# Performance work log

Hardware: AMD Instinct MI355X
Metric: run time of the kernel (lower is better)

Reference implementation:

```python
import jax, jax.numpy as jnp
import numpy as np

VALUES_PER_ITEM = 4  # 2-bit packed -> 4 values per uint8


def setup_inputs() -> dict:
    key = jax.random.key(0)
    k1, k2, k3 = jax.random.split(key, 3)
    x = jax.random.normal(k1, (4, 4096, 2048), dtype=jnp.float32)
    # packed uint8 weights, stored as int32 with values in [0, 256)
    weight_packed = jax.random.randint(k2, (512, 2048), 0, 256, dtype=jnp.int32)
    weight_scale = jnp.ones((1,), dtype=jnp.float32)
    bias = jax.random.normal(k3, (2048,), dtype=jnp.float32) * 0.01
    return {"x": x, "weight_packed": weight_packed,
            "weight_scale": weight_scale, "bias": bias}


def unpack_weights_bitnet(packed, dtype):
    # packed: [out//4, in]. HF BitNet layout: group i occupies rows
    # [i*out//4 : (i+1)*out//4], extracted from bits (2i, 2i+1), minus 1.
    parts = [((packed >> (2 * i)) & 3) for i in range(VALUES_PER_ITEM)]
    return jnp.concatenate(parts, axis=0).astype(dtype) - 1.0  # [out, in]


def activation_quant(x, num_bits=8):
    qn = -(2 ** (num_bits - 1))          # -128
    qp = 2 ** (num_bits - 1) - 1         # 127
    amax = jnp.clip(jnp.max(jnp.abs(x), axis=-1, keepdims=True), 1e-5, None)
    scale = qp / amax                    # per-token scale, [..., 1]
    # round-half-to-even matches torch .round(); keep in float (int8-valued)
    xq = jnp.clip(jnp.round(x * scale), qn, qp)
    return xq, scale


def reference(x, weight_packed, weight_scale, bias):
    w = unpack_weights_bitnet(weight_packed, x.dtype)  # [out, in]
    xq, in_scale = activation_quant(x)                 # [b,s,in], [b,s,1]
    y = jnp.einsum('bsd,od->bso', xq, w)               # int8-valued GEMM in fp
    y = y / (weight_scale * in_scale)                  # rescale
    return y + bias
```

## Files before the change

kernel.cpp:

```cpp
#include <hip/hip_runtime.h>
#include <stdint.h>


typedef __attribute__((ext_vector_type(4)))  int int4v;
typedef __attribute__((ext_vector_type(16))) int int16v;

#define GLOBAL_AS __attribute__((address_space(1)))
#define LDS_AS    __attribute__((address_space(3)))

static constexpr int MK = 2048;
static constexpr int NN = 2048;
static constexpr int MM = 16384;

__global__ void quant_kernel(const float* __restrict__ x,
                             const float* __restrict__ wscale,
                             signed char* __restrict__ xq,
                             float* __restrict__ rf) {
    const int m = blockIdx.x;
    const int t = threadIdx.x;
    const float4* xr = (const float4*)(x + (size_t)m * MK);
    float4 v0 = xr[t];
    float4 v1 = xr[t + 256];
    float amax = fmaxf(fmaxf(fabsf(v0.x), fabsf(v0.y)),
                       fmaxf(fabsf(v0.z), fabsf(v0.w)));
    amax = fmaxf(amax, fmaxf(fmaxf(fabsf(v1.x), fabsf(v1.y)),
                             fmaxf(fabsf(v1.z), fabsf(v1.w))));
    #pragma unroll
    for (int off = 32; off >= 1; off >>= 1)
        amax = fmaxf(amax, __shfl_xor(amax, off));
    __shared__ float smax[4];
    if ((t & 63) == 0) smax[t >> 6] = amax;
    __syncthreads();
    float a0 = fmaxf(fmaxf(smax[0], smax[1]), fmaxf(smax[2], smax[3]));
    a0 = fmaxf(a0, 1e-5f);
    const float scale = 127.0f / a0;
    if (t == 0) rf[m] = a0 / (127.0f * wscale[0]);

    auto q = [&](float f) -> int {
        float r = rintf(f * scale);
        r = fminf(fmaxf(r, -128.0f), 127.0f);
        return (int)r;
    };
    int p0 = (q(v0.x) & 255) | ((q(v0.y) & 255) << 8) |
             ((q(v0.z) & 255) << 16) | ((q(v0.w) & 255) << 24);
    int p1 = (q(v1.x) & 255) | ((q(v1.y) & 255) << 8) |
             ((q(v1.z) & 255) << 16) | ((q(v1.w) & 255) << 24);
    int* xqr = (int*)(xq + (size_t)m * MK);
    xqr[t]       = p0;
    xqr[t + 256] = p1;
}

__global__ void unpack_kernel(const int* __restrict__ packed,
                              signed char* __restrict__ W) {
    const int idx = blockIdx.x * 256 + threadIdx.x;
    const int r  = idx >> 9;
    const int kq = idx & 511;
    const int4 p = ((const int4*)packed)[idx];
    int* Wi = (int*)W;
    #pragma unroll
    for (int i = 0; i < 4; i++) {
        const int sh = 2 * i;
        int b0 = ((((p.x >> sh) & 3) - 1) & 255);
        int b1 = ((((p.y >> sh) & 3) - 1) & 255);
        int b2 = ((((p.z >> sh) & 3) - 1) & 255);
        int b3 = ((((p.w >> sh) & 3) - 1) & 255);
        Wi[(i * 512 + r) * 512 + kq] = b0 | (b1 << 8) | (b2 << 16) | (b3 << 24);
    }
}

#define WAITV(N) asm volatile("s_waitcnt vmcnt(" #N ")" ::: "memory")
#define BAR() do { __builtin_amdgcn_s_barrier(); \
                   __builtin_amdgcn_sched_barrier(0); } while (0)

__device__ __forceinline__ void stage_half(const signed char* __restrict__ src,
                                           int row0, int k0, int h, int ss,
                                           unsigned char* plane,
                                           int wave, int lane) {
    const int csrc = (((lane & 7) ^ (lane >> 3)) << 4);
    #pragma unroll
    for (int j = 0; j < 2; ++j) {
        const int rw = wave * 16 + j * 8 + (lane >> 3);
        const int r  = (rw & ((1 << ss) - 1)) + (h << ss)
                     + ((rw >> ss) << (ss + 1));
        const signed char* ga = src + (size_t)(row0 + r) * MK + k0 + csrc;
        __builtin_amdgcn_global_load_lds((const GLOBAL_AS void*)ga,
            (LDS_AS void*)(plane + (h << 14) + (wave * 2 + j) * 1024),
            16, 0, 0);
    }
}

#define RD_A(MH)                                                               \
  _Pragma("unroll")                                                            \
  for (int mt = 0; mt < 2; ++mt)                                               \
    _Pragma("unroll")                                                          \
    for (int ks = 0; ks < 4; ++ks)                                             \
      a[mt][ks] = *(const int4v*)(shp + cb + (MH)*16384 + arow + mt*4096       \
                                  + cbyte[ks]);

#define RD_B(NH, breg)                                                         \
  _Pragma("unroll")                                                            \
  for (int ks = 0; ks < 4; ++ks)                                               \
    breg[ks] = *(const int4v*)(shp + cb + brow + (NH)*16384 + cbyte[ks]);

#define MFM(MH, NH, breg)                                                      \
  do {                                                                         \
    __builtin_amdgcn_s_setprio(1);                                             \
    _Pragma("unroll")                                                          \
    for (int mt = 0; mt < 2; ++mt)                                             \
      _Pragma("unroll")                                                        \
      for (int ks = 0; ks < 4; ++ks)                                           \
        acc[(MH)*2+mt][NH] = __builtin_amdgcn_mfma_i32_32x32x32_i8(            \
            a[mt][ks], breg[ks], acc[(MH)*2+mt][NH], 0, 0, 0);                 \
    __builtin_amdgcn_s_setprio(0);                                             \
  } while (0)

__global__ void __launch_bounds__(512, 2)
gemm_kernel(const signed char* __restrict__ xq,
            const signed char* __restrict__ W,
            const float* __restrict__ rf,
            const float* __restrict__ bias,
            float* __restrict__ out) {
    __shared__ __attribute__((aligned(16))) unsigned char sh[131072];
    unsigned char* shp = sh;

    const int tid  = threadIdx.x;
    const int wave = tid >> 6;
    const int lane = tid & 63;
    const int wm = wave >> 2;
    const int wn = wave & 3;

    const int bs = ((blockIdx.x & 7) << 6) | (blockIdx.x >> 3);
    const int m0 = (bs >> 3) << 8;
    const int n0 = (bs & 7) << 8;

    const int ar = lane & 31, hl = lane >> 5;
    int cbyte[4];
    #pragma unroll
    for (int ks = 0; ks < 4; ++ks)
        cbyte[ks] = ((((ks << 1) | hl) ^ (ar & 7)) << 4);
    const int arow = (wm * 64 + ar) * 128;
    const int brow = 32768 + (wn * 32 + ar) * 128;

    int4v a[2][4], b0[4], b1[4];
    int16v acc[4][2] = {};

    stage_half(xq, m0, 0, 0, 6, shp,         wave, lane);
    stage_half(W,  n0, 0, 0, 5, shp + 32768, wave, lane);
    stage_half(W,  n0, 0, 1, 5, shp + 32768, wave, lane);
    stage_half(xq, m0, 0, 1, 6, shp,         wave, lane);
    WAITV(4);
    BAR();

    #pragma unroll 1
    for (int t = 0; t < 15; ++t) {
        const int cb = (t & 1) << 16;
        const int nb = cb ^ 65536;
        const int k1 = (t + 1) << 7;

        RD_A(0); RD_B(0, b0);
        stage_half(xq, m0, k1, 0, 6, shp + nb,         wave, lane);
        WAITV(4); BAR();
        MFM(0, 0, b0);

        RD_B(1, b1);
        stage_half(W,  n0, k1, 0, 5, shp + nb + 32768, wave, lane);
        WAITV(4); BAR();
        MFM(0, 1, b1);

        RD_A(1);
        stage_half(W,  n0, k1, 1, 5, shp + nb + 32768, wave, lane);
        WAITV(6); BAR();
        MFM(1, 0, b0);

        stage_half(xq, m0, k1, 1, 6, shp + nb,         wave, lane);
        WAITV(4); BAR();
        MFM(1, 1, b1);
    }
    {
        const int cb = 65536;
        RD_A(0); RD_B(0, b0);
        WAITV(2); BAR();
        MFM(0, 0, b0);

        RD_B(1, b1);
        WAITV(0); BAR();
        MFM(0, 1, b1);

        RD_A(1);
        BAR();
        MFM(1, 0, b0);

        BAR();
        MFM(1, 1, b1);
    }

    const int nb0 = n0 + wn * 64 + ar;
    const float bva = bias[nb0];
    const float bvb = bias[nb0 + 32];
    #pragma unroll
    for (int MH = 0; MH < 2; ++MH) {
        #pragma unroll
        for (int mt = 0; mt < 2; ++mt) {
            const int mbase = m0 + wm * 128 + MH * 64 + mt * 32 + hl * 4;
            #pragma unroll
            for (int q = 0; q < 4; ++q) {
                #pragma unroll
                for (int rr = 0; rr < 4; ++rr) {
                    const int m = mbase + q * 8 + rr;
                    const float frm = rf[m];
                    float* orow = out + (size_t)m * NN;
                    orow[nb0]      = (float)acc[MH*2+mt][0][q*4+rr] * frm + bva;
                    orow[nb0 + 32] = (float)acc[MH*2+mt][1][q*4+rr] * frm + bvb;
                }
            }
        }
    }
}

extern "C" void kernel_launch(void* const* d_in, const int* in_sizes, int n_in,
                              void* d_out, int out_size, void* d_ws, size_t ws_size,
                              hipStream_t stream) {
    const float* x      = (const float*)d_in[0];
    const int*   packed = (const int*)d_in[1];
    const float* wscale = (const float*)d_in[2];
    const float* bias   = (const float*)d_in[3];
    float* out = (float*)d_out;

    signed char* xq = (signed char*)d_ws;
    signed char* W  = xq + (size_t)MM * MK;
    float*       rf = (float*)(W + (size_t)NN * MK);

    quant_kernel<<<MM, 256, 0, stream>>>(x, wscale, xq, rf);
    unpack_kernel<<<(512 * 512) / 256, 256, 0, stream>>>(packed, W);
    gemm_kernel<<<dim3(512), 512, 0, stream>>>(xq, W, rf, bias, out);
}
```

Before: 290.1 us.

## Load W fragments directly from global to registers, halving LDS footprint

```diff
diff --git a/kernel.cpp b/kernel.cpp
--- a/kernel.cpp
+++ b/kernel.cpp
@@ -73,15 +73,14 @@
                    __builtin_amdgcn_sched_barrier(0); } while (0)
 
 __device__ __forceinline__ void stage_half(const signed char* __restrict__ src,
-                                           int row0, int k0, int h, int ss,
+                                           int row0, int k0, int h,
                                            unsigned char* plane,
                                            int wave, int lane) {
     const int csrc = (((lane & 7) ^ (lane >> 3)) << 4);
     #pragma unroll
     for (int j = 0; j < 2; ++j) {
         const int rw = wave * 16 + j * 8 + (lane >> 3);
-        const int r  = (rw & ((1 << ss) - 1)) + (h << ss)
-                     + ((rw >> ss) << (ss + 1));
+        const int r  = (rw & 63) + h * 64 + ((rw >> 6) << 7);
         const signed char* ga = src + (size_t)(row0 + r) * MK + k0 + csrc;
         __builtin_amdgcn_global_load_lds((const GLOBAL_AS void*)ga,
             (LDS_AS void*)(plane + (h << 14) + (wave * 2 + j) * 1024),
@@ -89,18 +88,18 @@
     }
 }
 
-#define RD_A(MH)                                                               \
-  _Pragma("unroll")                                                            \
-  for (int mt = 0; mt < 2; ++mt)                                               \
-    _Pragma("unroll")                                                          \
-    for (int ks = 0; ks < 4; ++ks)                                             \
-      a[mt][ks] = *(const int4v*)(shp + cb + (MH)*16384 + arow + mt*4096       \
+#define RD_A(MH, cb)                                                           \
+  _Pragma("unroll")                                                           \
+  for (int mt = 0; mt < 2; ++mt)                                              \
+    _Pragma("unroll")                                                         \
+    for (int ks = 0; ks < 4; ++ks)                                            \
+      a[mt][ks] = *(const int4v*)(shp + (cb) + (MH)*16384 + arow + mt*4096    \
                                   + cbyte[ks]);
 
-#define RD_B(NH, breg)                                                         \
-  _Pragma("unroll")                                                            \
-  for (int ks = 0; ks < 4; ++ks)                                               \
-    breg[ks] = *(const int4v*)(shp + cb + brow + (NH)*16384 + cbyte[ks]);
+#define LOADB(B, NH, k1)                                                       \
+  _Pragma("unroll")                                                           \
+  for (int ks = 0; ks < 4; ++ks)                                              \
+    B[NH][ks] = *(const int4v*)(bptr + (size_t)(NH) * 32 * MK + (k1) + ks*32);
 
 #define MFM(MH, NH, breg)                                                      \
   do {                                                                         \
@@ -114,13 +113,34 @@
     __builtin_amdgcn_s_setprio(0);                                             \
   } while (0)
 
+#define BODY(cb, nb, k1)                                                       \
+  do {                                                                         \
+                                                                      \
+    RD_A(0, cb);                                                               \
+    stage_half(xq, m0, (k1), 0, shp + (nb), wave, lane);                       \
+    LOADB(BN, 0, (k1));                                                        \
+    WAITV(12); __builtin_amdgcn_sched_barrier(0);                              \
+    MFM(0, 0, BC[0]);                                                          \
+                                                                      \
+    LOADB(BN, 1, (k1));                                                        \
+    WAITV(10); BAR();                                                          \
+    MFM(0, 1, BC[1]);                                                          \
+                                                                      \
+    RD_A(1, cb);                                                               \
+    stage_half(xq, m0, (k1), 1, shp + (nb), wave, lane);                       \
+    MFM(1, 0, BC[0]);                                                          \
+                                                                      \
+    WAITV(10); BAR();                                                          \
+    MFM(1, 1, BC[1]);                                                          \
+  } while (0)
+
 __global__ void __launch_bounds__(512, 2)
 gemm_kernel(const signed char* __restrict__ xq,
             const signed char* __restrict__ W,
             const float* __restrict__ rf,
             const float* __restrict__ bias,
             float* __restrict__ out) {
-    __shared__ __attribute__((aligned(16))) unsigned char sh[131072];
+    __shared__ __attribute__((aligned(16))) unsigned char sh[65536];
     unsigned char* shp = sh;
 
     const int tid  = threadIdx.x;
@@ -139,59 +159,50 @@
     for (int ks = 0; ks < 4; ++ks)
         cbyte[ks] = ((((ks << 1) | hl) ^ (ar & 7)) << 4);
     const int arow = (wm * 64 + ar) * 128;
-    const int brow = 32768 + (wn * 32 + ar) * 128;
-
-    int4v a[2][4], b0[4], b1[4];
+
+    const signed char* bptr = W + (size_t)(n0 + wn * 64 + ar) * MK + hl * 16;
+
+    int4v a[2][4];
+    int4v bX[2][4], bY[2][4];
     int16v acc[4][2] = {};
 
-    stage_half(xq, m0, 0, 0, 6, shp,         wave, lane);
-    stage_half(W,  n0, 0, 0, 5, shp + 32768, wave, lane);
-    stage_half(W,  n0, 0, 1, 5, shp + 32768, wave, lane);
-    stage_half(xq, m0, 0, 1, 6, shp,         wave, lane);
-    WAITV(4);
-    BAR();
+    stage_half(xq, m0, 0, 0, shp, wave, lane);
+    { LOADB(bX, 0, 0); }
+    { LOADB(bX, 1, 0); }
+    stage_half(xq, m0, 0, 1, shp, wave, lane);
+    WAITV(10); BAR();
 
     #pragma unroll 1
-    for (int t = 0; t < 15; ++t) {
-        const int cb = (t & 1) << 16;
-        const int nb = cb ^ 65536;
-        const int k1 = (t + 1) << 7;
-
-        RD_A(0); RD_B(0, b0);
-        stage_half(xq, m0, k1, 0, 6, shp + nb,         wave, lane);
-        WAITV(4); BAR();
-        MFM(0, 0, b0);
-
-        RD_B(1, b1);
-        stage_half(W,  n0, k1, 0, 5, shp + nb + 32768, wave, lane);
-        WAITV(4); BAR();
-        MFM(0, 1, b1);
-
-        RD_A(1);
-        stage_half(W,  n0, k1, 1, 5, shp + nb + 32768, wave, lane);
-        WAITV(6); BAR();
-        MFM(1, 0, b0);
-
-        stage_half(xq, m0, k1, 1, 6, shp + nb,         wave, lane);
-        WAITV(4); BAR();
-        MFM(1, 1, b1);
+    for (int tp = 0; tp < 7; ++tp) {
+        const int k1a = (2 * tp + 1) << 7;
+        const int k1b = (2 * tp + 2) << 7;
+        #define BC bX
+        #define BN bY
+        BODY(0, 32768, k1a);
+        #undef BC
+        #undef BN
+        #define BC bY
+        #define BN bX
+        BODY(32768, 0, k1b);
+        #undef BC
+        #undef BN
     }
     {
-        const int cb = 65536;
-        RD_A(0); RD_B(0, b0);
-        WAITV(2); BAR();
-        MFM(0, 0, b0);
-
-        RD_B(1, b1);
+        #define BC bX
+        #define BN bY
+        BODY(0, 32768, 15 << 7);
+        #undef BC
+        #undef BN
+    }
+    {
+        RD_A(0, 32768);
+        WAITV(6); __builtin_amdgcn_sched_barrier(0);
+        MFM(0, 0, bY[0]);
         WAITV(0); BAR();
-        MFM(0, 1, b1);
-
-        RD_A(1);
-        BAR();
-        MFM(1, 0, b0);
-
-        BAR();
-        MFM(1, 1, b1);
+        MFM(0, 1, bY[1]);
+        RD_A(1, 32768);
+        MFM(1, 0, bY[0]);
+        MFM(1, 1, bY[1]);
     }
 
     const int nb0 = n0 + wn * 64 + ar;
```

Result: slower. 324.7 us (+11.9%).
